# Kernel optimization log

Hardware: AMD Instinct MI355X
Metric: run time of the kernel (lower is better)

Reference implementation:

```python
import jax, jax.numpy as jnp
import numpy as np

B, C, Hh, Ww = 1, 64, 64, 64
NH, DK = 8, 64
D = NH * DK  # 512


def _gelu(x):
    return jax.nn.gelu(x, approximate=False)


def _dwconv3x3(x, w):
    # x: [b, ch, h, w]; w: [ch, 1, 3, 3] (torch depthwise layout, groups=ch)
    return jax.lax.conv_general_dilated(
        x, w, window_strides=(1, 1), padding='SAME',
        feature_group_count=x.shape[1],
        dimension_numbers=('NCHW', 'OIHW', 'NCHW'))


def _bn(x, g, b, m, v):
    # eval-mode BatchNorm2d, eps=1e-5
    s = (g / jnp.sqrt(v + 1e-5))[None, :, None, None]
    return (x - m[None, :, None, None]) * s + b[None, :, None, None]


def setup_inputs() -> dict:
    key = jax.random.key(0)
    ks = jax.random.split(key, 16)
    r = lambda k, sh, sc=0.02: (jax.random.normal(k, sh, dtype=jnp.float32) * sc)
    return {
        'x_in': jax.random.normal(ks[0], (B, C, Hh, Ww), dtype=jnp.float32),
        'Wq': r(ks[1], (D, C)), 'Wk': r(ks[2], (D, C)), 'Wv': r(ks[3], (D, C)),
        'scale': jnp.ones((NH, 1, 1), dtype=jnp.float32),
        'Wout': r(ks[4], (C, D)), 'bout': jnp.zeros((C,), jnp.float32),
        'dw_w': r(ks[5], (D, 1, 3, 3), 0.1), 'dw_b': jnp.zeros((D,), jnp.float32),
        'dw_g': jnp.ones((D,), jnp.float32), 'dw_bt': jnp.zeros((D,), jnp.float32),
        'dw_m': jnp.zeros((D,), jnp.float32), 'dw_v': jnp.ones((D,), jnp.float32),
        'ci_w1': r(ks[6], (D // 4, D)), 'ci_b1': jnp.zeros((D // 4,), jnp.float32),
        'ci_w2': r(ks[7], (D, D // 4)), 'ci_b2': jnp.zeros((D,), jnp.float32),
        'si_w1': r(ks[8], (D // 16, D)), 'si_b1': jnp.zeros((D // 16,), jnp.float32),
        'si_g': jnp.ones((D // 16,), jnp.float32), 'si_bt': jnp.zeros((D // 16,), jnp.float32),
        'si_m': jnp.zeros((D // 16,), jnp.float32), 'si_v': jnp.ones((D // 16,), jnp.float32),
        'si_w2': r(ks[9], (1, D // 16)), 'si_b2': jnp.zeros((1,), jnp.float32),
        'pe_w1': r(ks[10], (C, 1, 3, 3), 0.1), 'pe_w2': r(ks[11], (C, 1, 3, 3), 0.1),
    }


def reference(x_in, Wq, Wk, Wv, scale, Wout, bout,
              dw_w, dw_b, dw_g, dw_bt, dw_m, dw_v,
              ci_w1, ci_b1, ci_w2, ci_b2,
              si_w1, si_b1, si_g, si_bt, si_m, si_v, si_w2, si_b2,
              pe_w1, pe_w2):
    b, c, h, w = x_in.shape
    n = h * w
    nh, dk = NH, DK
    dh = nh * dk

    x = x_in.reshape(b, c, n).transpose(0, 2, 1)  # [b, n, c]

    q = (x @ Wq.T).reshape(b, n, nh, dk).transpose(0, 2, 1, 3)  # [b,nh,n,dk]
    k = (x @ Wk.T).reshape(b, n, nh, dk).transpose(0, 2, 1, 3)
    v_flat = x @ Wv.T                                            # [b,n,D]
    v = v_flat.reshape(b, n, nh, dk).transpose(0, 2, 1, 3)
    v_img = v_flat.transpose(0, 2, 1).reshape(b, dh, h, w)       # [b,D,h,w]

    # cosine normalization (F.normalize, eps=1e-12)
    q = q / jnp.clip(jnp.linalg.norm(q, axis=-1, keepdims=True), 1e-12)
    k = k / jnp.clip(jnp.linalg.norm(k, axis=-1, keepdims=True), 1e-12)

    dist = jnp.einsum('bhid,bhjd->bhij', q, k) * scale  # scale: [nh,1,1] broadcast
    dist = jax.nn.softmax(dist, axis=-1)
    att = jnp.einsum('bhij,bhjd->bhid', dist, v)          # [b,nh,n,dk]
    att = att.transpose(0, 2, 1, 3).reshape(b, n, dh)     # [b,n,D]

    # depthwise conv branch on v
    conv_x = _gelu(_bn(_dwconv3x3(v_img, dw_w) + dw_b[None, :, None, None],
                       dw_g, dw_bt, dw_m, dw_v))          # [b,D,h,w]

    # channel interaction: global-avg-pool of attention, two 1x1 convs
    pooled = att.mean(axis=1)                             # [b,D] (avg over n == avg over h,w)
    cm = _gelu(pooled @ ci_w1.T + ci_b1) @ ci_w2.T + ci_b2  # [b,D]

    # spatial interaction: 1x1 -> BN -> GELU -> 1x1 on conv branch
    s1 = jnp.einsum('bdhw,ed->behw', conv_x, si_w1) + si_b1[None, :, None, None]
    s1 = _gelu(_bn(s1, si_g, si_bt, si_m, si_v))
    sm = jnp.einsum('behw,oe->bohw', s1, si_w2) + si_b2[None, :, None, None]  # [b,1,h,w]
    sm = sm.transpose(0, 2, 3, 1).reshape(b, n, 1)

    attened = att * jax.nn.sigmoid(sm)
    conv_g = conv_x * jax.nn.sigmoid(cm)[:, :, None, None]
    conv_g = conv_g.transpose(0, 2, 3, 1).reshape(b, n, dh)

    y = (attened + conv_g) @ Wout.T + bout               # [b,n,c]
    out = y.reshape(b, c, h, w)  # faithful to original (no transpose before reshape)

    embed = _dwconv3x3(_gelu(_dwconv3x3(x_in, pe_w1)), pe_w2)
    return out + embed
```

## Files before the change

kernel.cpp:

```cpp
#include <hip/hip_runtime.h>


#define LOG2E 1.442695040888963f

typedef __attribute__((ext_vector_type(8))) short bf16x8;
typedef __attribute__((ext_vector_type(4))) float f32x4;
typedef __attribute__((ext_vector_type(4))) int i32x4;
typedef __attribute__((ext_vector_type(2))) int i32x2;
typedef __attribute__((ext_vector_type(4))) ushort u16x4;

__device__ __forceinline__ ushort f2bf(float x){
  uint u = __float_as_uint(x);
  u += 0x7fffu + ((u >> 16) & 1u);
  return (ushort)(u >> 16);
}
__device__ __forceinline__ float bf2f(ushort h){
  return __uint_as_float(((uint)h) << 16);
}
__device__ __forceinline__ float gelu_(float x){
  return 0.5f * x * (1.0f + erff(x * 0.70710678118654752f));
}
__device__ __forceinline__ float sigmoid_(float x){
  return 1.0f / (1.0f + __expf(-x));
}
__device__ __forceinline__ float exp2_(float x){
  float r; asm("v_exp_f32 %0, %1" : "=v"(r) : "v"(x)); return r;
}
__device__ __forceinline__ int cvtpk(float lo, float hi){
  int r; asm("v_cvt_pk_bf16_f32 %0, %1, %2" : "=v"(r) : "v"(lo), "v"(hi)); return r;
}
__device__ __forceinline__ bf16x8 packf8(const float* s){
  f32x4 x0 = *(const f32x4*)s;
  f32x4 x1 = *(const f32x4*)(s+4);
  union{ i32x4 i; bf16x8 v; } u;
  u.i[0]=cvtpk(x0[0],x0[1]); u.i[1]=cvtpk(x0[2],x0[3]);
  u.i[2]=cvtpk(x1[0],x1[1]); u.i[3]=cvtpk(x1[2],x1[3]);
  return u.v;
}
__device__ __forceinline__ void gload16(const ushort* g, ushort* l){
  __builtin_amdgcn_global_load_lds(
    (const __attribute__((address_space(1))) uint*)(const void*)g,
    (__attribute__((address_space(3))) uint*)(void*)l, 16, 0, 0);
}

__global__ __launch_bounds__(256) void k_qkv(const float* __restrict__ xin,
    const float* __restrict__ Wq, const float* __restrict__ Wk,
    const float* __restrict__ Wv, const float* __restrict__ scale,
    ushort* __restrict__ q_bf, ushort* __restrict__ k_bf, ushort* __restrict__ vT,
    const float* __restrict__ pe_w1, const float* __restrict__ pe_w2,
    float* __restrict__ embed, const float* __restrict__ Wout,
    const float* __restrict__ si_w1, ushort* __restrict__ Woutb,
    ushort* __restrict__ si_w1b, float* __restrict__ pooled){
  __shared__ float t0[20*64];
  __shared__ float t1[18*64];
  const int tid = threadIdx.x;
  if (blockIdx.y == 1){
    if (tid < 192){
      int i = blockIdx.x*192 + tid;
      if (i < 32768) Woutb[i] = f2bf(Wout[i]);
      else           si_w1b[i - 32768] = f2bf(si_w1[i - 32768]);
    }
    if (blockIdx.x == 0){ pooled[tid] = 0.f; pooled[tid+256] = 0.f; }
    const int c = blockIdx.x >> 2;
    const int r0 = (blockIdx.x & 3) * 16;
    const float* src = xin + (size_t)c*4096;
#pragma unroll
    for (int i=0;i<5;i++){
      int idx = tid + 256*i;
      if (idx < 1280){
        int lr = idx >> 6, x = idx & 63;
        int gr = r0 - 2 + lr;
        t0[idx] = (gr >= 0 && gr < 64) ? src[gr*64 + x] : 0.f;
      }
    }
    __syncthreads();
    float w1[9], w2[9];
#pragma unroll
    for (int i=0;i<9;i++){ w1[i] = pe_w1[c*9+i]; w2[i] = pe_w2[c*9+i]; }
#pragma unroll
    for (int i=0;i<5;i++){
      int idx = tid + 256*i;
      if (idx < 1152){
        int lr = idx >> 6, x = idx & 63;
        int gr = r0 - 1 + lr;
        float acc = 0.f;
        if (gr >= 0 && gr < 64){
#pragma unroll
          for (int ky=0;ky<3;ky++){
            int gy = gr + ky - 1;
            if (gy < 0 || gy > 63) continue;
#pragma unroll
            for (int kx=0;kx<3;kx++){
              int xx = x + kx - 1;
              if (xx < 0 || xx > 63) continue;
              acc += w1[ky*3+kx] * t0[(lr + ky)*64 + xx];
            }
          }
          acc = gelu_(acc);
        }
        t1[idx] = acc;
      }
    }
    __syncthreads();
    float* dst = embed + (size_t)c*4096;
#pragma unroll
    for (int i=0;i<4;i++){
      int idx = tid + 256*i;
      int lr = idx >> 6, x = idx & 63;
      int gr = r0 + lr;
      float acc = 0.f;
#pragma unroll
      for (int ky=0;ky<3;ky++){
        int gy = gr + ky - 1;
        if (gy < 0 || gy > 63) continue;
#pragma unroll
        for (int kx=0;kx<3;kx++){
          int xx = x + kx - 1;
          if (xx < 0 || xx > 63) continue;
          acc += w2[ky*3+kx] * t1[(lr + ky)*64 + xx];
        }
      }
      dst[gr*64 + x] = acc;
    }
    return;
  }
  const int n0 = blockIdx.x * 16;
  const int lane = tid & 63, w = tid >> 6;
  const int l15 = lane & 15, g = lane >> 4;
  const int obase = w * 128;
  const int n = n0 + l15;
  float xa[8], xc[8];
#pragma unroll
  for (int j=0;j<8;j++){
    xa[j] = xin[(8*g + j)*4096 + n];
    xc[j] = xin[(32 + 8*g + j)*4096 + n];
  }
  union{ i32x4 i; bf16x8 v; } ua, uc;
  ua.i[0]=cvtpk(xa[0],xa[1]); ua.i[1]=cvtpk(xa[2],xa[3]);
  ua.i[2]=cvtpk(xa[4],xa[5]); ua.i[3]=cvtpk(xa[6],xa[7]);
  uc.i[0]=cvtpk(xc[0],xc[1]); uc.i[1]=cvtpk(xc[2],xc[3]);
  uc.i[2]=cvtpk(xc[4],xc[5]); uc.i[3]=cvtpk(xc[6],xc[7]);
  const bf16x8 a0 = ua.v, a1 = uc.v;
  const float* Ws[3] = { Wq, Wk, Wv };
  for (int z=0; z<3; ++z){
    const float* W = Ws[z];
    f32x4 acc[8];
#pragma unroll
    for (int t=0;t<8;t++) acc[t] = (f32x4){0.f,0.f,0.f,0.f};
#pragma unroll
    for (int t=0;t<8;t++){
      const float* brow = W + (size_t)(obase + 16*t + l15)*64;
      bf16x8 b0 = packf8(brow + 8*g);
      bf16x8 b1 = packf8(brow + 32 + 8*g);
      acc[t] = __builtin_amdgcn_mfma_f32_16x16x32_bf16(a0, b0, acc[t], 0,0,0);
      acc[t] = __builtin_amdgcn_mfma_f32_16x16x32_bf16(a1, b1, acc[t], 0,0,0);
    }
    if (z < 2){
#pragma unroll
      for (int hh=0; hh<2; hh++){
        float sfac = (z==0) ? (scale[2*w+hh] * LOG2E) : 1.0f;
#pragma unroll
        for (int r=0;r<4;r++){
          float ss = 0.f;
#pragma unroll
          for (int tt=0;tt<4;tt++){ float v = acc[hh*4+tt][r]; ss += v*v; }
          ss += __shfl_xor(ss, 1); ss += __shfl_xor(ss, 2);
          ss += __shfl_xor(ss, 4); ss += __shfl_xor(ss, 8);
          float inv = sfac / fmaxf(sqrtf(ss), 1e-12f);
#pragma unroll
          for (int tt=0;tt<4;tt++) acc[hh*4+tt][r] *= inv;
        }
      }
      ushort* dst = (z==0) ? q_bf : k_bf;
#pragma unroll
      for (int t=0;t<8;t++){
        int col = obase + 16*t + l15;
#pragma unroll
        for (int r=0;r<4;r++)
          dst[(size_t)(n0 + 4*g + r)*512 + col] = f2bf(acc[t][r]);
      }
    } else {
#pragma unroll
      for (int t=0;t<8;t++){
        int col = obase + 16*t + l15;
        u16x4 vs;
#pragma unroll
        for (int r=0;r<4;r++) vs[r] = f2bf(acc[t][r]);
        *(u16x4*)(vT + (size_t)col*4096 + n0 + 4*g) = vs;
      }
    }
  }
}

__global__ __launch_bounds__(512) void k_attn_conv(const ushort* __restrict__ q_bf,
    const ushort* __restrict__ k_bf, const ushort* __restrict__ vT,
    ushort* __restrict__ O_part, float* __restrict__ lsum_part, int log2S,
    const float* __restrict__ dw_w, const float* __restrict__ dw_b,
    const float* __restrict__ dw_g, const float* __restrict__ dw_bt,
    const float* __restrict__ dw_m, const float* __restrict__ dw_v,
    ushort* __restrict__ conv_x){
  __shared__ ushort Kt[2][4096];
  __shared__ ushort Vt[2][4096];
  const int S = 1 << log2S;
  const int NA = 128 << log2S;
  const int bid = blockIdx.x;
  const int tid = threadIdx.x;

  if (bid >= NA){
    float* tile = (float*)&Kt[0][0];
    const int d = bid - NA;
    const ushort* src = vT + (size_t)d*4096;
#pragma unroll
    for (int j=0;j<2;j++){
      u16x4 va = *(const u16x4*)(src + tid*4 + 2048*j);
      f32x4 vf;
#pragma unroll
      for (int i=0;i<4;i++) vf[i] = bf2f(va[i]);
      *(f32x4*)&tile[tid*4 + 2048*j] = vf;
    }
    __syncthreads();
    float wv[9];
#pragma unroll
    for (int i=0;i<9;i++) wv[i] = dw_w[d*9+i];
    const float bias = dw_b[d];
    const float bnsc = dw_g[d] * rsqrtf(dw_v[d] + 1e-5f);
    const float bnb  = dw_bt[d] - dw_m[d]*bnsc;
    ushort* dst = conv_x + (size_t)d*4096;
#pragma unroll 4
    for (int i=0;i<8;i++){
      int p = tid + 512*i;
      int y = p >> 6, x = p & 63;
      float acc = 0.f;
#pragma unroll
      for (int ky=0;ky<3;ky++){
        int yy = y + ky - 1;
        if (yy < 0 || yy > 63) continue;
#pragma unroll
        for (int kx=0;kx<3;kx++){
          int xx = x + kx - 1;
          if (xx < 0 || xx > 63) continue;
          acc += wv[ky*3+kx] * tile[yy*64 + xx];
        }
      }
      float cc = (acc + bias)*bnsc + bnb;
      dst[p] = f2bf(gelu_(cc));
    }
    return;
  }
  const int combo = bid & (8*S - 1);
  const int qb = bid >> (3 + log2S);
  const int h = combo >> log2S;
  const int seg = combo & (S - 1);
  const int kv0 = seg * (4096 >> log2S);
  const int iters = (4096 >> log2S) >> 6;
  const int lane = tid & 63, w = tid >> 6;
  const int l15 = lane & 15, g = lane >> 4;

  const int lr8 = lane >> 3;
  const int swzc = ((lane & 7) ^ lr8) << 3;
  const ushort* kSrc = k_bf + (size_t)(kv0 + w*8 + lr8)*512 + h*64 + swzc;
  const ushort* vSrc = vT + (size_t)(h*64 + w*8 + lr8)*4096 + kv0 + swzc;
  ushort* klds[2] = { &Kt[0][w*512], &Kt[1][w*512] };
  ushort* vlds[2] = { &Vt[0][w*512], &Vt[1][w*512] };

  const int qrow0 = qb*256 + w*32;
  bf16x8 qa[2][2];
#pragma unroll
  for (int tq=0;tq<2;tq++){
    const ushort* qrow = q_bf + (size_t)(qrow0 + tq*16 + l15)*512 + h*64;
    qa[tq][0] = *(const bf16x8*)(qrow + 8*g);
    qa[tq][1] = *(const bf16x8*)(qrow + 32 + 8*g);
  }
  f32x4 O[2][4];
#pragma unroll
  for (int tq=0;tq<2;tq++)
#pragma unroll
    for (int t=0;t<4;t++) O[tq][t] = (f32x4){0.f,0.f,0.f,0.f};
  float lsum[2] = {0.f,0.f};

  gload16(kSrc, klds[0]);
  gload16(vSrc, vlds[0]);
  asm volatile("s_waitcnt vmcnt(0)" ::: "memory");
  __builtin_amdgcn_s_barrier();

  const int x7 = l15 & 7;
  const int g2 = g >> 1, gh = (g & 1) << 2;

  for (int it = 0; it < iters; ++it){
    const int buf = it & 1;
    if (it + 1 < iters){
      kSrc += 64*512; vSrc += 64;
      gload16(kSrc, klds[buf^1]);
      gload16(vSrc, vlds[buf^1]);
    }
    const ushort* Kb = Kt[buf];
    const ushort* Vb = Vt[buf];
    i32x4 PA[2][2];
#pragma unroll
    for (int s=0;s<4;s++){
      const int rr = 16*s + l15;
      bf16x8 kf0 = *(const bf16x8*)&Kb[rr*64 + ((g     ^ x7) << 3)];
      bf16x8 kf1 = *(const bf16x8*)&Kb[rr*64 + (((4+g) ^ x7) << 3)];
      const int sp = s >> 1, hi = (s & 1) << 1;
#pragma unroll
      for (int tq=0;tq<2;tq++){
        f32x4 st = (f32x4){0.f,0.f,0.f,0.f};
        st = __builtin_amdgcn_mfma_f32_16x16x32_bf16(kf0, qa[tq][0], st, 0,0,0);
        st = __builtin_amdgcn_mfma_f32_16x16x32_bf16(kf1, qa[tq][1], st, 0,0,0);
        float p0 = exp2_(st[0]), p1 = exp2_(st[1]);
        float p2 = exp2_(st[2]), p3 = exp2_(st[3]);
        lsum[tq] += (p0 + p1) + (p2 + p3);
        PA[tq][sp][hi]   = cvtpk(p0, p1);
        PA[tq][sp][hi+1] = cvtpk(p2, p3);
      }
    }
    __builtin_amdgcn_s_setprio(1);
#pragma unroll
    for (int t=0;t<4;t++){
      const int rr = 16*t + l15;
      union { bf16x8 v; i32x2 h2[2]; } u0, u1;
      u0.h2[0] = *(const i32x2*)&Vb[rr*64 + ((g2       ^ x7) << 3) + gh];
      u0.h2[1] = *(const i32x2*)&Vb[rr*64 + (((2 + g2) ^ x7) << 3) + gh];
      u1.h2[0] = *(const i32x2*)&Vb[rr*64 + (((4 + g2) ^ x7) << 3) + gh];
      u1.h2[1] = *(const i32x2*)&Vb[rr*64 + (((6 + g2) ^ x7) << 3) + gh];
#pragma unroll
      for (int tq=0;tq<2;tq++){
        union { i32x4 i; bf16x8 v; } a0, a1;
        a0.i = PA[tq][0]; a1.i = PA[tq][1];
        O[tq][t] = __builtin_amdgcn_mfma_f32_16x16x32_bf16(a0.v, u0.v, O[tq][t], 0,0,0);
        O[tq][t] = __builtin_amdgcn_mfma_f32_16x16x32_bf16(a1.v, u1.v, O[tq][t], 0,0,0);
      }
    }
    __builtin_amdgcn_s_setprio(0);
    asm volatile("s_waitcnt vmcnt(0)" ::: "memory");
    __builtin_amdgcn_s_barrier();
  }
#pragma unroll
  for (int tq=0;tq<2;tq++){
    float ls = lsum[tq];
    ls += __shfl_xor(ls, 16); ls += __shfl_xor(ls, 32);
    if (g == 0)
      lsum_part[((size_t)seg*8 + h)*4096 + qrow0 + tq*16 + l15] = ls;
  }
  ushort* Op = O_part + (size_t)seg*4096*512;
#pragma unroll
  for (int tq=0;tq<2;tq++)
#pragma unroll
    for (int t=0;t<4;t++)
#pragma unroll
      for (int r=0;r<4;r++)
        Op[(size_t)(qrow0 + tq*16 + 4*g + r)*512 + h*64 + 16*t + l15] = f2bf(O[tq][t][r]);
}

template<int S>
__global__ __launch_bounds__(256) void k_comb_t(const ushort* __restrict__ O_part,
    const float* __restrict__ lsum_part, ushort* __restrict__ att_bf,
    float* __restrict__ pooled){
  __shared__ float Linv[16][8];
  __shared__ float red[4][512];
  const int qbase = blockIdx.x * 16;
  const int tid = threadIdx.x;
  if (tid < 128){
    int q = tid >> 3, h = tid & 7;
    float L = 0.f;
#pragma unroll
    for (int s=0;s<S;s++) L += lsum_part[((size_t)s*8 + h)*4096 + qbase + q];
    Linv[q][h] = 1.0f / L;
  }
  __syncthreads();
  const int ch = tid & 63;
  const int qg = tid >> 6;
  const int d0 = ch * 8;
  const int hh = ch >> 3;
  float pool[8] = {0.f,0.f,0.f,0.f,0.f,0.f,0.f,0.f};
#pragma unroll
  for (int qq=0; qq<4; qq++){
    const int q = qg*4 + qq;
    const size_t idx = (size_t)(qbase + q)*512 + d0;
    i32x4 seg[S];
#pragma unroll
    for (int s=0;s<S;s++)
      seg[s] = *(const i32x4*)(O_part + (size_t)s*4096*512 + idx);
    float o[8];
#pragma unroll
    for (int j=0;j<8;j++){
      uint pk = ((const uint*)&seg[0])[j>>1];
      o[j] = bf2f((ushort)(pk >> ((j&1)*16)));
    }
#pragma unroll
    for (int s=1;s<S;s++)
#pragma unroll
      for (int j=0;j<8;j++){
        uint pk = ((const uint*)&seg[s])[j>>1];
        o[j] += bf2f((ushort)(pk >> ((j&1)*16)));
      }
    const float li = Linv[q][hh];
    union{ i32x4 i; } w;
#pragma unroll
    for (int j=0;j<8;j++){ o[j] *= li; pool[j] += o[j]; }
    w.i[0]=cvtpk(o[0],o[1]); w.i[1]=cvtpk(o[2],o[3]);
    w.i[2]=cvtpk(o[4],o[5]); w.i[3]=cvtpk(o[6],o[7]);
    *(i32x4*)(att_bf + idx) = w.i;
  }
  *(f32x4*)&red[qg][d0]     = *(f32x4*)&pool[0];
  *(f32x4*)&red[qg][d0 + 4] = *(f32x4*)&pool[4];
  __syncthreads();
  {
    int d = tid;
    float s0 = red[0][d] + red[1][d] + red[2][d] + red[3][d];
    int d2 = tid + 256;
    float s1 = red[0][d2] + red[1][d2] + red[2][d2] + red[3][d2];
    atomicAdd(&pooled[d], s0);
    atomicAdd(&pooled[d2], s1);
  }
}

__global__ __launch_bounds__(512) void k_final(const ushort* __restrict__ att_bf,
    const ushort* __restrict__ conv_x, const ushort* __restrict__ si_w1b,
    const float* __restrict__ si_b1, const float* __restrict__ si_g,
    const float* __restrict__ si_bt, const float* __restrict__ si_m,
    const float* __restrict__ si_v, const float* __restrict__ si_w2,
    const float* __restrict__ si_b2,
    const float* __restrict__ pooled, const float* __restrict__ ci_w1,
    const float* __restrict__ ci_b1, const float* __restrict__ ci_w2,
    const float* __restrict__ ci_b2,
    const ushort* __restrict__ Woutb, const float* __restrict__ bout,
    const float* __restrict__ embed, float* __restrict__ out){
  __shared__ ushort ct[16*520];
  __shared__ float pl[512];
  __shared__ float h1[128];
  __shared__ float scm[512];
  __shared__ f32x4 part2[8][2][64];
  __shared__ float smv[16];
  __shared__ f32x4 part[8][4][64];
  const int tid = threadIdx.x;
  const int lane = tid & 63, w = tid >> 6;
  const int l15 = lane & 15, g = lane >> 4;
  const int n0 = blockIdx.x * 16;
  const int rowA = n0 + l15;
  pl[tid] = pooled[tid] * (1.0f/4096.0f);
  {
    const ushort* s = conv_x + (size_t)tid*4096 + n0;
    union{ i32x4 q[2]; ushort e[16]; } u;
    u.q[0] = *(const i32x4*)s;
    u.q[1] = *(const i32x4*)(s + 8);
#pragma unroll
    for (int j=0;j<16;j++) ct[j*520 + tid] = u.e[j];
  }
  bf16x8 at8[2];
#pragma unroll
  for (int kk=0;kk<2;kk++){
    int k0 = w*64 + kk*32 + 8*g;
    at8[kk] = *(const bf16x8*)(att_bf + (size_t)rowA*512 + k0);
  }
  __syncthreads();
  {
    int e = tid >> 2;
    int base = (tid & 3) * 128;
    float acc = 0.f;
    const float* wr = ci_w1 + (size_t)e*512 + base;
#pragma unroll 8
    for (int c=0;c<128;c++) acc += wr[c]*pl[base + c];
    acc += __shfl_xor(acc, 1);
    acc += __shfl_xor(acc, 2);
    if (!(tid & 3)) h1[e] = gelu_(acc + ci_b1[e]);
  }
  bf16x8 cn8[2];
#pragma unroll
  for (int kk=0;kk<2;kk++){
    int k0 = w*64 + kk*32 + 8*g;
    cn8[kk] = *(const bf16x8*)&ct[l15*520 + k0];
  }
  __syncthreads();
  {
    float acc = ci_b2[tid];
    const float* wr = ci_w2 + (size_t)tid*128;
#pragma unroll 8
    for (int e=0;e<128;e++) acc += wr[e]*h1[e];
    scm[tid] = sigmoid_(acc);
  }
  f32x4 a2[2];
  a2[0] = (f32x4){0.f,0.f,0.f,0.f};
  a2[1] = (f32x4){0.f,0.f,0.f,0.f};
#pragma unroll
  for (int kk=0;kk<2;kk++){
    int k0 = w*64 + kk*32 + 8*g;
#pragma unroll
    for (int t=0;t<2;t++){
      bf16x8 b = *(const bf16x8*)(si_w1b + (size_t)(16*t + l15)*512 + k0);
      a2[t] = __builtin_amdgcn_mfma_f32_16x16x32_bf16(cn8[kk], b, a2[t], 0,0,0);
    }
  }
  part2[w][0][lane] = a2[0];
  part2[w][1][lane] = a2[1];
  __syncthreads();
  if (w == 0){
    float rowv[4] = {0.f,0.f,0.f,0.f};
#pragma unroll
    for (int t=0;t<2;t++){
      f32x4 s4 = part2[0][t][lane];
#pragma unroll
      for (int ww=1;ww<8;ww++) s4 = s4 + part2[ww][t][lane];
      int e = 16*t + l15;
      float s = si_g[e] * rsqrtf(si_v[e] + 1e-5f);
      float b1 = si_b1[e] - si_m[e];
      float bt = si_bt[e];
      float w2e = si_w2[e];
#pragma unroll
      for (int r=0;r<4;r++){
        float v = (s4[r] + b1)*s + bt;
        rowv[r] += w2e * gelu_(v);
      }
    }
    float sb2 = si_b2[0];
#pragma unroll
    for (int r=0;r<4;r++){
      float v = rowv[r];
      v += __shfl_xor(v,1); v += __shfl_xor(v,2);
      v += __shfl_xor(v,4); v += __shfl_xor(v,8);
      if (l15 == 0) smv[4*g + r] = sigmoid_(v + sb2);
    }
  }
  __syncthreads();
  const float srow = smv[l15];
  f32x4 acc[4];
#pragma unroll
  for (int t=0;t<4;t++) acc[t] = (f32x4){0.f,0.f,0.f,0.f};
#pragma unroll
  for (int kk=0;kk<2;kk++){
    int k0 = w*64 + kk*32 + 8*g;
    bf16x8 af;
#pragma unroll
    for (int i=0;i<8;i++){
      int d = k0 + i;
      float zv = bf2f((ushort)at8[kk][i]) * srow + bf2f((ushort)cn8[kk][i]) * scm[d];
      af[i] = (short)f2bf(zv);
    }
#pragma unroll
    for (int t=0;t<4;t++){
      bf16x8 bf8 = *(const bf16x8*)(Woutb + (size_t)(16*t+l15)*512 + k0);
      acc[t] = __builtin_amdgcn_mfma_f32_16x16x32_bf16(af, bf8, acc[t], 0,0,0);
    }
  }
#pragma unroll
  for (int t=0;t<4;t++) part[w][t][lane] = acc[t];
  __syncthreads();
  if (w < 4){
    f32x4 s4 = part[0][w][lane];
#pragma unroll
    for (int ww=1;ww<8;ww++) s4 = s4 + part[ww][w][lane];
    int o = 16*w + l15;
    float bo = bout[o];
#pragma unroll
    for (int r=0;r<4;r++){
      int row = n0 + 4*g + r;
      size_t idx = (size_t)row*64 + o;
      out[idx] = s4[r] + bo + embed[idx];
    }
  }
}

extern "C" void kernel_launch(void* const* d_in, const int* in_sizes, int n_in,
                              void* d_out, int out_size, void* d_ws, size_t ws_size,
                              hipStream_t stream){
  (void)in_sizes; (void)n_in; (void)out_size;
  const float* x_in  = (const float*)d_in[0];
  const float* Wq    = (const float*)d_in[1];
  const float* Wk    = (const float*)d_in[2];
  const float* Wv    = (const float*)d_in[3];
  const float* scale = (const float*)d_in[4];
  const float* Wout  = (const float*)d_in[5];
  const float* bout  = (const float*)d_in[6];
  const float* dw_w  = (const float*)d_in[7];
  const float* dw_b  = (const float*)d_in[8];
  const float* dw_g  = (const float*)d_in[9];
  const float* dw_bt = (const float*)d_in[10];
  const float* dw_m  = (const float*)d_in[11];
  const float* dw_v  = (const float*)d_in[12];
  const float* ci_w1 = (const float*)d_in[13];
  const float* ci_b1 = (const float*)d_in[14];
  const float* ci_w2 = (const float*)d_in[15];
  const float* ci_b2 = (const float*)d_in[16];
  const float* si_w1 = (const float*)d_in[17];
  const float* si_b1 = (const float*)d_in[18];
  const float* si_g  = (const float*)d_in[19];
  const float* si_bt = (const float*)d_in[20];
  const float* si_m  = (const float*)d_in[21];
  const float* si_v  = (const float*)d_in[22];
  const float* si_w2 = (const float*)d_in[23];
  const float* si_b2 = (const float*)d_in[24];
  const float* pe_w1 = (const float*)d_in[25];
  const float* pe_w2 = (const float*)d_in[26];
  float* out = (float*)d_out;

  char* p = (char*)d_ws;
  auto alloc = [&](size_t bytes)->char*{
    char* r = p; p += (bytes + 255) & ~(size_t)255; return r;
  };
  ushort* q_bf    = (ushort*)alloc((size_t)4096*512*2);
  ushort* k_bf    = (ushort*)alloc((size_t)4096*512*2);
  ushort* vTb     = (ushort*)alloc((size_t)512*4096*2);
  ushort* att_bf  = (ushort*)alloc((size_t)4096*512*2);
  ushort* conv_x  = (ushort*)alloc((size_t)512*4096*2);
  ushort* Woutb   = (ushort*)alloc((size_t)32768*2);
  ushort* si_w1b  = (ushort*)alloc((size_t)16384*2);
  float*  embed   = (float*) alloc((size_t)64*4096*4);
  float*  lsum_p  = (float*) alloc((size_t)8*8*4096*4);
  float*  pooled  = (float*) alloc(512*4);
  size_t used = (size_t)(p - (char*)d_ws);
  size_t segBytes = (size_t)4096*512*2 + 256;
  size_t avail = (ws_size > used) ? (ws_size - used) : 0;
  int log2S = 2;
  if (avail < 4*segBytes) log2S = 1;
  if (avail < 2*segBytes) log2S = 0;
  int S = 1 << log2S;
  ushort* O_part = (ushort*)alloc((size_t)S*segBytes);
  int NA = 128 << log2S;

  k_qkv<<<dim3(256,2), 256, 0, stream>>>(x_in, Wq, Wk, Wv, scale, q_bf, k_bf, vTb,
                                         pe_w1, pe_w2, embed, Wout, si_w1,
                                         Woutb, si_w1b, pooled);
  k_attn_conv<<<NA + 512, 512, 0, stream>>>(q_bf, k_bf, vTb, O_part, lsum_p, log2S,
                                            dw_w, dw_b, dw_g, dw_bt, dw_m, dw_v,
                                            conv_x);
  if (log2S == 2)
    k_comb_t<4><<<256, 256, 0, stream>>>(O_part, lsum_p, att_bf, pooled);
  else if (log2S == 1)
    k_comb_t<2><<<256, 256, 0, stream>>>(O_part, lsum_p, att_bf, pooled);
  else
    k_comb_t<1><<<256, 256, 0, stream>>>(O_part, lsum_p, att_bf, pooled);
  k_final<<<256, 512, 0, stream>>>(att_bf, conv_x, si_w1b, si_b1, si_g, si_bt,
                                   si_m, si_v, si_w2, si_b2,
                                   pooled, ci_w1, ci_b1, ci_w2, ci_b2,
                                   Woutb, bout, embed, out);
}
```

Measured before the change: 100.8 us.

## Double the attention KV tile to 128 rows per iteration

```diff
diff --git a/kernel.cpp b/kernel.cpp
--- a/kernel.cpp
+++ b/kernel.cpp
@@ -199,8 +199,8 @@
     const float* __restrict__ dw_g, const float* __restrict__ dw_bt,
     const float* __restrict__ dw_m, const float* __restrict__ dw_v,
     ushort* __restrict__ conv_x){
-  __shared__ ushort Kt[2][4096];
-  __shared__ ushort Vt[2][4096];
+  __shared__ ushort Kt[2][8192];
+  __shared__ ushort Vt[2][8192];
   const int S = 1 << log2S;
   const int NA = 128 << log2S;
   const int bid = blockIdx.x;
@@ -252,16 +252,24 @@
   const int h = combo >> log2S;
   const int seg = combo & (S - 1);
   const int kv0 = seg * (4096 >> log2S);
-  const int iters = (4096 >> log2S) >> 6;
+  const int iters = (4096 >> log2S) >> 7;
   const int lane = tid & 63, w = tid >> 6;
   const int l15 = lane & 15, g = lane >> 4;
 
   const int lr8 = lane >> 3;
-  const int swzc = ((lane & 7) ^ lr8) << 3;
-  const ushort* kSrc = k_bf + (size_t)(kv0 + w*8 + lr8)*512 + h*64 + swzc;
-  const ushort* vSrc = vT + (size_t)(h*64 + w*8 + lr8)*4096 + kv0 + swzc;
-  ushort* klds[2] = { &Kt[0][w*512], &Kt[1][w*512] };
-  ushort* vlds[2] = { &Vt[0][w*512], &Vt[1][w*512] };
+  const int swzcK = ((lane & 7) ^ lr8) << 3;
+  const ushort* kSrc0 = k_bf + (size_t)(kv0 + w*16 + lr8)*512 + h*64 + swzcK;
+  const ushort* kSrc1 = kSrc0 + (size_t)8*512;
+  const int vr0 = w*8 + (lane >> 4);
+  const int vr1 = vr0 + 4;
+  const ushort* vSrc0 = vT + (size_t)(h*64 + vr0)*4096 + kv0
+                        + (((lane & 15) ^ (vr0 & 7)) << 3);
+  const ushort* vSrc1 = vT + (size_t)(h*64 + vr1)*4096 + kv0
+                        + (((lane & 15) ^ (vr1 & 7)) << 3);
+  ushort* kl0[2] = { &Kt[0][(w*16)*64],   &Kt[1][(w*16)*64] };
+  ushort* kl1[2] = { &Kt[0][(w*16+8)*64], &Kt[1][(w*16+8)*64] };
+  ushort* vl0[2] = { &Vt[0][(w*8)*128],   &Vt[1][(w*8)*128] };
+  ushort* vl1[2] = { &Vt[0][(w*8+4)*128], &Vt[1][(w*8+4)*128] };
 
   const int qrow0 = qb*256 + w*32;
   bf16x8 qa[2][2];
@@ -278,60 +286,60 @@
     for (int t=0;t<4;t++) O[tq][t] = (f32x4){0.f,0.f,0.f,0.f};
   float lsum[2] = {0.f,0.f};
 
-  gload16(kSrc, klds[0]);
-  gload16(vSrc, vlds[0]);
+  gload16(kSrc0, kl0[0]); gload16(kSrc1, kl1[0]);
+  gload16(vSrc0, vl0[0]); gload16(vSrc1, vl1[0]);
   asm volatile("s_waitcnt vmcnt(0)" ::: "memory");
   __builtin_amdgcn_s_barrier();
 
   const int x7 = l15 & 7;
-  const int g2 = g >> 1, gh = (g & 1) << 2;
+  const int gq = g >> 1, gh2 = (g & 1) << 2;
 
   for (int it = 0; it < iters; ++it){
     const int buf = it & 1;
     if (it + 1 < iters){
-      kSrc += 64*512; vSrc += 64;
-      gload16(kSrc, klds[buf^1]);
-      gload16(vSrc, vlds[buf^1]);
+      kSrc0 += 128*512; kSrc1 += 128*512; vSrc0 += 128; vSrc1 += 128;
+      gload16(kSrc0, kl0[buf^1]); gload16(kSrc1, kl1[buf^1]);
+      gload16(vSrc0, vl0[buf^1]); gload16(vSrc1, vl1[buf^1]);
     }
     const ushort* Kb = Kt[buf];
     const ushort* Vb = Vt[buf];
-    i32x4 PA[2][2];
-#pragma unroll
-    for (int s=0;s<4;s++){
-      const int rr = 16*s + l15;
-      bf16x8 kf0 = *(const bf16x8*)&Kb[rr*64 + ((g     ^ x7) << 3)];
-      bf16x8 kf1 = *(const bf16x8*)&Kb[rr*64 + (((4+g) ^ x7) << 3)];
-      const int sp = s >> 1, hi = (s & 1) << 1;
-#pragma unroll
-      for (int tq=0;tq<2;tq++){
-        f32x4 st = (f32x4){0.f,0.f,0.f,0.f};
-        st = __builtin_amdgcn_mfma_f32_16x16x32_bf16(kf0, qa[tq][0], st, 0,0,0);
-        st = __builtin_amdgcn_mfma_f32_16x16x32_bf16(kf1, qa[tq][1], st, 0,0,0);
-        float p0 = exp2_(st[0]), p1 = exp2_(st[1]);
-        float p2 = exp2_(st[2]), p3 = exp2_(st[3]);
-        lsum[tq] += (p0 + p1) + (p2 + p3);
-        PA[tq][sp][hi]   = cvtpk(p0, p1);
-        PA[tq][sp][hi+1] = cvtpk(p2, p3);
-      }
-    }
-    __builtin_amdgcn_s_setprio(1);
-#pragma unroll
-    for (int t=0;t<4;t++){
-      const int rr = 16*t + l15;
-      union { bf16x8 v; i32x2 h2[2]; } u0, u1;
-      u0.h2[0] = *(const i32x2*)&Vb[rr*64 + ((g2       ^ x7) << 3) + gh];
-      u0.h2[1] = *(const i32x2*)&Vb[rr*64 + (((2 + g2) ^ x7) << 3) + gh];
-      u1.h2[0] = *(const i32x2*)&Vb[rr*64 + (((4 + g2) ^ x7) << 3) + gh];
-      u1.h2[1] = *(const i32x2*)&Vb[rr*64 + (((6 + g2) ^ x7) << 3) + gh];
-#pragma unroll
-      for (int tq=0;tq<2;tq++){
-        union { i32x4 i; bf16x8 v; } a0, a1;
-        a0.i = PA[tq][0]; a1.i = PA[tq][1];
-        O[tq][t] = __builtin_amdgcn_mfma_f32_16x16x32_bf16(a0.v, u0.v, O[tq][t], 0,0,0);
-        O[tq][t] = __builtin_amdgcn_mfma_f32_16x16x32_bf16(a1.v, u1.v, O[tq][t], 0,0,0);
-      }
-    }
-    __builtin_amdgcn_s_setprio(0);
+#pragma unroll
+    for (int ks=0; ks<4; ++ks){
+      i32x4 PA[2];
+#pragma unroll
+      for (int s2=0; s2<2; ++s2){
+        const int rr = 16*(2*ks + s2) + l15;
+        bf16x8 kf0 = *(const bf16x8*)&Kb[rr*64 + ((g     ^ x7) << 3)];
+        bf16x8 kf1 = *(const bf16x8*)&Kb[rr*64 + (((4+g) ^ x7) << 3)];
+        const int hi = s2 << 1;
+#pragma unroll
+        for (int tq=0; tq<2; ++tq){
+          f32x4 st = (f32x4){0.f,0.f,0.f,0.f};
+          st = __builtin_amdgcn_mfma_f32_16x16x32_bf16(kf0, qa[tq][0], st, 0,0,0);
+          st = __builtin_amdgcn_mfma_f32_16x16x32_bf16(kf1, qa[tq][1], st, 0,0,0);
+          float p0 = exp2_(st[0]), p1 = exp2_(st[1]);
+          float p2 = exp2_(st[2]), p3 = exp2_(st[3]);
+          lsum[tq] += (p0 + p1) + (p2 + p3);
+          PA[tq][hi]   = cvtpk(p0, p1);
+          PA[tq][hi+1] = cvtpk(p2, p3);
+        }
+      }
+      __builtin_amdgcn_s_setprio(1);
+#pragma unroll
+      for (int t=0;t<4;++t){
+        const int rr = 16*t + l15;
+        const int c0 = 4*ks + gq, c1 = 4*ks + 2 + gq;
+        union { bf16x8 v; i32x2 h2[2]; } u;
+        u.h2[0] = *(const i32x2*)&Vb[rr*128 + ((c0 ^ x7) << 3) + gh2];
+        u.h2[1] = *(const i32x2*)&Vb[rr*128 + ((c1 ^ x7) << 3) + gh2];
+#pragma unroll
+        for (int tq=0;tq<2;++tq){
+          union { i32x4 i; bf16x8 v; } a; a.i = PA[tq];
+          O[tq][t] = __builtin_amdgcn_mfma_f32_16x16x32_bf16(a.v, u.v, O[tq][t], 0,0,0);
+        }
+      }
+      __builtin_amdgcn_s_setprio(0);
+    }
     asm volatile("s_waitcnt vmcnt(0)" ::: "memory");
     __builtin_amdgcn_s_barrier();
   }
```

Measured after the change: 112.0 us. +11.1%, slower.
